# Kernel tuning notes

Measured on AMD Instinct MI355X. Metric: run time of the kernel, lower is better.

Reference implementation:

```python
import jax, jax.numpy as jnp
import numpy as np

N, E = 50000, 800000
D_IN, HID, H, C, E_DIM = 128, 128, 4, 32, 32  # C = HID // H


def setup_inputs() -> dict:
    key = jax.random.key(0)
    ks = jax.random.split(key, 16)
    def lin(k, fan_in, fan_out):
        return jax.random.normal(k, (fan_in, fan_out), jnp.float32) / np.sqrt(fan_in)
    return {
        "x": jax.random.normal(ks[0], (N, D_IN), jnp.float32),
        "edge_index": jax.random.randint(ks[1], (2, E), 0, N, jnp.int32),
        "edge_attr": jax.random.normal(ks[2], (E, E_DIM), jnp.float32),
        # TransformerConv params (bias=True on q/k/v and skip; lin_edge has no bias in PyG)
        "Wq": lin(ks[3], D_IN, HID), "bq": jnp.zeros((HID,), jnp.float32),
        "Wk": lin(ks[4], D_IN, HID), "bk": jnp.zeros((HID,), jnp.float32),
        "Wv": lin(ks[5], D_IN, HID), "bv": jnp.zeros((HID,), jnp.float32),
        "We": lin(ks[6], E_DIM, HID),
        "Wskip": lin(ks[7], D_IN, HID), "bskip": jnp.zeros((HID,), jnp.float32),
        # MLP([HID, HID, HID]) -> two Linear layers, GELU(tanh) after each (plain_last=False)
        "W1": lin(ks[8], HID, HID), "b1": jnp.zeros((HID,), jnp.float32),
        "W2": lin(ks[9], HID, HID), "b2": jnp.zeros((HID,), jnp.float32),
    }


def reference(x, edge_index, edge_attr, Wq, bq, Wk, bk, Wv, bv, We, Wskip, bskip, W1, b1, W2, b2):
    src, dst = edge_index[0], edge_index[1]  # messages flow src(j) -> dst(i)
    n = x.shape[0]
    q = (x @ Wq + bq).reshape(n, H, C)
    k = (x @ Wk + bk).reshape(n, H, C)
    v = (x @ Wv + bv).reshape(n, H, C)
    e = (edge_attr @ We).reshape(-1, H, C)          # [E,H,C]
    kj = k[src] + e                                  # gather + edge lift
    vj = v[src] + e
    alpha = jnp.einsum("ehc,ehc->eh", q[dst], kj) / np.sqrt(C)  # [E,H]
    # segment softmax over destination neighborhoods (PyG softmax semantics)
    amax = jax.ops.segment_max(alpha, dst, num_segments=n)      # [N,H]
    amax = jnp.where(jnp.isfinite(amax), amax, 0.0)
    ex = jnp.exp(alpha - amax[dst])
    denom = jax.ops.segment_sum(ex, dst, num_segments=n)
    alpha = ex / (denom[dst] + 1e-16)
    # (attention dropout p=0.3 is inactive in eval mode)
    agg = jax.ops.segment_sum(vj * alpha[:, :, None], dst, num_segments=n)  # [N,H,C]
    out = agg.reshape(n, HID) + (x @ Wskip + bskip)  # concat heads + root skip
    # residual MLP: gelu(tanh) after every layer since plain_last=False, norm=None
    h = jax.nn.gelu(out @ W1 + b1, approximate=True)
    h = jax.nn.gelu(h @ W2 + b2, approximate=True)
    return out + h
```

## Files before the change

### kernel.cpp

```cpp
#include <hip/hip_runtime.h>
#include <math.h>


#define D 128
#define EDIM 32

using bf16x8 = __attribute__((ext_vector_type(8))) short;
using f32x4  = __attribute__((ext_vector_type(4))) float;
using ushort8 = __attribute__((ext_vector_type(8))) unsigned short;
using v2h = __attribute__((ext_vector_type(2))) _Float16;

__device__ inline unsigned short f2bf(float f) {
    unsigned int u = __float_as_uint(f);
    u += 0x7FFFu + ((u >> 16) & 1u);
    return (unsigned short)(u >> 16);
}
__device__ inline float bf2f(unsigned short h) {
    return __uint_as_float(((unsigned int)h) << 16);
}
__device__ inline unsigned short f2h(float f) {
    union { _Float16 h; unsigned short u; } c;
    c.h = (_Float16)f;
    return c.u;
}
__device__ inline v2h u2h(unsigned int u) {
    union { unsigned int x; v2h h; } c; c.x = u; return c.h;
}
__device__ inline float gelu_fast(float x) {
    float x3 = x * x * x;
    float u = 0.7978845608028654f * (x + 0.044715f * x3);
    float t = 1.f - 2.f / (__expf(2.f * u) + 1.f);
    return 0.5f * x * (1.f + t);
}
__device__ inline float quad_add(float x) {
    int a = __builtin_amdgcn_update_dpp(0, __float_as_int(x), 0xB1, 0xF, 0xF, true);
    x += __int_as_float(a);
    a = __builtin_amdgcn_update_dpp(0, __float_as_int(x), 0x4E, 0xF, 0xF, true);
    x += __int_as_float(a);
    return x;
}

__device__ inline bf16x8 ldsB(const unsigned short* sw, int col, int kk0) {
    return *(const bf16x8*)(sw + col * 128 + (kk0 ^ ((col & 7) << 3)));
}

__global__ __launch_bounds__(256) void prep_kernel(
    const float* __restrict__ Wq, const float* __restrict__ Wk,
    const float* __restrict__ Wv, const float* __restrict__ Wsk,
    const float* __restrict__ W1, const float* __restrict__ W2,
    const float* __restrict__ We, const float* __restrict__ bq,
    unsigned short* __restrict__ Wt, float* __restrict__ bqE,
    const int* __restrict__ EI, int* __restrict__ deg, int E, int HB,
    const float* __restrict__ x, unsigned short* __restrict__ XB, long xtot)
{
    if ((int)blockIdx.x >= 513 + HB) {
        long i8 = ((long)(blockIdx.x - 513 - HB) * 256 + threadIdx.x) * 8;
        if (i8 + 8 <= xtot) {
            float4 a = *(const float4*)(x + i8);
            float4 b = *(const float4*)(x + i8 + 4);
            ushort8 u;
            u[0] = f2bf(a.x); u[1] = f2bf(a.y); u[2] = f2bf(a.z); u[3] = f2bf(a.w);
            u[4] = f2bf(b.x); u[5] = f2bf(b.y); u[6] = f2bf(b.z); u[7] = f2bf(b.w);
            *(ushort8*)(XB + i8) = u;
        }
        return;
    }
    if (blockIdx.x >= 513) {
        int e = (blockIdx.x - 513) * 256 + threadIdx.x;
        if (e < E) atomicAdd(&deg[EI[E + e]], 1);
        return;
    }
    int t = blockIdx.x * 256 + threadIdx.x;
    int m = t >> 14;
    int r = t & 16383;
    if (m >= 8) {
        if (r < 128) {
            const int hb = r & 96, k = r & 31;
            const float* wek = We + (size_t)k * D + hb;
            float s = 0.f;
#pragma unroll 8
            for (int c = 0; c < 32; ++c) s = fmaf(bq[hb + c], wek[c], s);
            bqE[r] = s;
        }
        return;
    }
    int col = r & 127, kk = r >> 7;
    float v;
    if (m < 6) {
        const float* W = (m == 0) ? Wq : (m == 1) ? Wk : (m == 2) ? Wv
                       : (m == 3) ? Wsk : (m == 4) ? W1 : W2;
        v = W[(size_t)kk * D + col];
    } else if (m == 6) {
        const int hb = col & 96;
        const float* wqr = Wq + (size_t)kk * D + hb;
        const float* wer = We + (size_t)(col & 31) * D + hb;
        float s = 0.f;
#pragma unroll 8
        for (int c = 0; c < 32; ++c) s = fmaf(wqr[c], wer[c], s);
        v = s;
    } else {
        v = ((kk >> 5) == (col >> 5)) ? We[(size_t)(kk & 31) * D + col] : 0.f;
    }
    Wt[(size_t)m * 16384 + (size_t)col * 128 + (kk ^ ((col & 7) << 3))] = f2bf(v);
}

__global__ __launch_bounds__(1024) void scanA(
    const int* __restrict__ deg, int* __restrict__ rowptr,
    int* __restrict__ psums, int N)
{
    __shared__ int tmp[1024];
    const int t = threadIdx.x;
    const int i = blockIdx.x * 1024 + t;
    int v = (i < N) ? deg[i] : 0;
    tmp[t] = v;
    __syncthreads();
    for (int off = 1; off < 1024; off <<= 1) {
        int add = (t >= off) ? tmp[t - off] : 0;
        __syncthreads();
        tmp[t] += add;
        __syncthreads();
    }
    if (i < N) rowptr[i + 1] = tmp[t];
    if (t == 1023) psums[blockIdx.x] = tmp[1023];
}

__global__ __launch_bounds__(1024) void scanB(int* __restrict__ psums, int nb)
{
    __shared__ int tmp[1024];
    const int t = threadIdx.x;
    int v = (t < nb) ? psums[t] : 0;
    tmp[t] = v;
    __syncthreads();
    for (int off = 1; off < 1024; off <<= 1) {
        int add = (t >= off) ? tmp[t - off] : 0;
        __syncthreads();
        tmp[t] += add;
        __syncthreads();
    }
    if (t < nb) psums[t] = tmp[t] - v;
}

__global__ __launch_bounds__(256) void scanC(
    int* __restrict__ rowptr, int* __restrict__ cursor,
    const int* __restrict__ psums, int N)
{
    int i = blockIdx.x * 256 + threadIdx.x;
    if (i == 0) { rowptr[0] = 0; cursor[0] = 0; }
    if (i < N) {
        int val = rowptr[i + 1] + psums[i >> 10];
        rowptr[i + 1] = val;
        if (i + 1 < N) cursor[i + 1] = val;
    }
}

__global__ __launch_bounds__(256) void scatter_ea(
    const int* __restrict__ EI, const float* __restrict__ EA,
    int* __restrict__ cursor, int2* __restrict__ SE,
    unsigned short* __restrict__ EAH, int E)
{
    int e = blockIdx.x * 256 + threadIdx.x;
    if (e >= E) return;
    int src = EI[e];
    int dst = EI[E + e];

    const float4* s4 = (const float4*)(EA + (size_t)e * EDIM);
    unsigned short* op = EAH + (size_t)e * EDIM;
#pragma unroll
    for (int j = 0; j < 4; ++j) {
        float4 a = s4[2 * j], b = s4[2 * j + 1];
        ushort8 u;
        u[0] = f2h(a.x); u[1] = f2h(a.y); u[2] = f2h(a.z); u[3] = f2h(a.w);
        u[4] = f2h(b.x); u[5] = f2h(b.y); u[6] = f2h(b.z); u[7] = f2h(b.w);
        *(ushort8*)(op + j * 8) = u;
    }

    int pos = atomicAdd(&cursor[dst], 1);
    SE[pos] = make_int2(src, e);
}

__global__ __launch_bounds__(256) void gemm5(
    const unsigned short* __restrict__ XB, const unsigned short* __restrict__ Wt,
    const float* __restrict__ bq, const float* __restrict__ bk,
    const float* __restrict__ bv, const float* __restrict__ bs,
    const float* __restrict__ bqE,
    unsigned short* __restrict__ QA, unsigned short* __restrict__ KV,
    float* __restrict__ S, int N, int NB2)
{
    __shared__ unsigned short sw[16384];
    const int t = threadIdx.x;
    const int bid = blockIdx.x;
    const int m = bid / NB2;
    const int bx = bid - m * NB2;
    const int widx = (m < 4) ? m : 6;
    const int lane = t & 63;
    const int w = t >> 6;
    const int row0 = bx * 128 + w * 32;
    const int lrow = lane & 15;
    const int kb = (lane >> 4) * 8;
    const int rq = (lane >> 4) * 4;

    const unsigned short* gsrc = Wt + (size_t)widx * 16384;
    ushort8 stg[8];
#pragma unroll
    for (int it = 0; it < 8; ++it)
        stg[it] = *(const ushort8*)(gsrc + (t + it * 256) * 8);

    bf16x8 af0[4], af1[4];
    {
        int a0 = row0 + lrow;      if (a0 > N - 1) a0 = N - 1;
        int a1 = row0 + 16 + lrow; if (a1 > N - 1) a1 = N - 1;
        const unsigned short* x0 = XB + (size_t)a0 * D + kb;
        const unsigned short* x1 = XB + (size_t)a1 * D + kb;
#pragma unroll
        for (int kf = 0; kf < 4; ++kf) {
            af0[kf] = *(const bf16x8*)(x0 + kf * 32);
            af1[kf] = *(const bf16x8*)(x1 + kf * 32);
        }
    }

#pragma unroll
    for (int it = 0; it < 8; ++it)
        *(ushort8*)(&sw[(t + it * 256) * 8]) = stg[it];
    __syncthreads();

    const float* bias = (m == 0) ? bq : (m == 1) ? bk : (m == 2) ? bv
                      : (m == 3) ? bs : bqE;
    f32x4 acc0[8], acc1[8];
#pragma unroll
    for (int nf = 0; nf < 8; ++nf) {
        acc0[nf] = (f32x4){0.f, 0.f, 0.f, 0.f};
        acc1[nf] = (f32x4){0.f, 0.f, 0.f, 0.f};
    }
#pragma unroll
    for (int nf = 0; nf < 8; ++nf) {
        const int col = nf * 16 + lrow;
#pragma unroll
        for (int kf = 0; kf < 4; ++kf) {
            bf16x8 bfr = ldsB(sw, col, kf * 32 + kb);
            acc0[nf] = __builtin_amdgcn_mfma_f32_16x16x32_bf16(af0[kf], bfr, acc0[nf], 0, 0, 0);
            acc1[nf] = __builtin_amdgcn_mfma_f32_16x16x32_bf16(af1[kf], bfr, acc1[nf], 0, 0, 0);
        }
    }

    if (m == 3) {
#pragma unroll
        for (int rb = 0; rb < 2; ++rb) {
#pragma unroll
            for (int nf = 0; nf < 8; ++nf) {
                const int col = nf * 16 + lrow;
                const float bb = bias[col];
#pragma unroll
                for (int i = 0; i < 4; ++i) {
                    int r = row0 + rb * 16 + rq + i;
                    if (r < N)
                        S[(size_t)r * D + col] = ((rb == 0) ? acc0[nf][i] : acc1[nf][i]) + bb;
                }
            }
        }
        return;
    }

    __syncthreads();
#pragma unroll
    for (int rb = 0; rb < 2; ++rb) {
#pragma unroll
        for (int nf = 0; nf < 8; ++nf) {
            const int col = nf * 16 + lrow;
            const float bb = bias[col];
#pragma unroll
            for (int i = 0; i < 4; ++i)
                sw[(w * 32 + rb * 16 + rq + i) * 128 + col] =
                    f2h(((rb == 0) ? acc0[nf][i] : acc1[nf][i]) + bb);
        }
    }
    unsigned short* gout = (m == 0) ? QA : (m == 1) ? KV
                         : (m == 2) ? KV + 128 : QA + 128;
#pragma unroll
    for (int it = 0; it < 8; ++it) {
        const int gidx = it * 64 + lane;
        const int row_l = gidx >> 4;
        const int chk = gidx & 15;
        const int r = row0 + row_l;
        ushort8 vv = *(const ushort8*)(&sw[(w * 32 + row_l) * 128 + chk * 8]);
        if (r < N) *(ushort8*)(gout + (size_t)r * 256 + chk * 8) = vv;
    }
}

__global__ __launch_bounds__(256) void gather_pass(
    const int* __restrict__ rowptr, const int2* __restrict__ SE,
    const unsigned short* __restrict__ EAH,
    const unsigned short* __restrict__ QA, const unsigned short* __restrict__ KV,
    float* __restrict__ SB, unsigned short* __restrict__ SAS, int N)
{
    const int lane = threadIdx.x & 63;
    const int wid = threadIdx.x >> 6;
    const int n = blockIdx.x * 4 + wid;
    if (n >= N) return;
    const int g = lane & 15;
    const int grp = lane >> 4;
    const int eoff = (g & 3) * 8;

    v2h q2[4], qe2[4];
    {
        uint4 qr  = *(const uint4*)(QA + (size_t)n * 256 + g * 8);
        uint4 qer = *(const uint4*)(QA + (size_t)n * 256 + 128 + g * 8);
        q2[0] = u2h(qr.x);  q2[1] = u2h(qr.y);  q2[2] = u2h(qr.z);  q2[3] = u2h(qr.w);
        qe2[0] = u2h(qer.x); qe2[1] = u2h(qer.y); qe2[2] = u2h(qer.z); qe2[3] = u2h(qer.w);
    }

    const v2h zero2 = {(_Float16)0.f, (_Float16)0.f};
    v2h acc2[4], sa2[4];
#pragma unroll
    for (int i = 0; i < 4; ++i) { acc2[i] = zero2; sa2[i] = zero2; }
    float den = 0.f;

    const int i0 = rowptr[n], i1 = rowptr[n + 1];

    int2 se[4];
#pragma unroll
    for (int u = 0; u < 4; ++u) {
        int ii = i0 + grp + u * 4;
        se[u] = (ii < i1) ? SE[ii] : make_int2(-1, 0);
    }

    for (int base = i0; base < i1; base += 16) {
        unsigned int kr[4][4], vr[4][4], er[4][4];
#pragma unroll
        for (int u = 0; u < 4; ++u) {
            if (se[u].x >= 0) {
                const unsigned short* kv = KV + (size_t)se[u].x * 256 + g * 8;
                *(uint4*)kr[u] = *(const uint4*)(kv);
                *(uint4*)vr[u] = *(const uint4*)(kv + 128);
                *(uint4*)er[u] = *(const uint4*)(EAH + (size_t)se[u].y * EDIM + eoff);
            } else {
                *(uint4*)kr[u] = (uint4){0, 0, 0, 0};
                *(uint4*)vr[u] = (uint4){0, 0, 0, 0};
                *(uint4*)er[u] = (uint4){0, 0, 0, 0};
            }
        }
        int2 seN[4];
#pragma unroll
        for (int u = 0; u < 4; ++u) {
            int ii = base + 16 + grp + u * 4;
            seN[u] = (ii < i1) ? SE[ii] : make_int2(-1, 0);
        }
#pragma unroll
        for (int u = 0; u < 4; ++u) {
            v2h ps = zero2;
#pragma unroll
            for (int i = 0; i < 4; ++i) {
                ps += q2[i]  * u2h(kr[u][i]);
                ps += qe2[i] * u2h(er[u][i]);
            }
            float p = (float)ps[0] + (float)ps[1];
            p = quad_add(p);
            const float ex = (se[u].x >= 0) ? __expf(p * 0.17677669529663689f) : 0.f;
            den += ex;
            const _Float16 exh = (_Float16)ex;
            const v2h ex2 = {exh, exh};
#pragma unroll
            for (int i = 0; i < 4; ++i) {
                acc2[i] += ex2 * u2h(vr[u][i]);
                sa2[i]  += ex2 * u2h(er[u][i]);
            }
        }
#pragma unroll
        for (int u = 0; u < 4; ++u) se[u] = seN[u];
    }

    float acc[8], sa[8];
#pragma unroll
    for (int i = 0; i < 4; ++i) {
        acc[2 * i] = (float)acc2[i][0]; acc[2 * i + 1] = (float)acc2[i][1];
        sa[2 * i]  = (float)sa2[i][0];  sa[2 * i + 1]  = (float)sa2[i][1];
    }
#pragma unroll
    for (int off = 16; off <= 32; off <<= 1) {
        den += __shfl_xor(den, off, 64);
#pragma unroll
        for (int j = 0; j < 8; ++j) {
            acc[j] += __shfl_xor(acc[j], off, 64);
            sa[j]  += __shfl_xor(sa[j],  off, 64);
        }
    }

    if (grp == 0) {
        const float rden = 1.f / (den + 1e-16f);
        float* so = SB + (size_t)n * D + g * 8;
        unsigned short* po = SAS + (size_t)n * D + g * 8;
#pragma unroll
        for (int j = 0; j < 8; ++j) {
            so[j] = fmaf(acc[j], rden, so[j]);
            po[j] = f2bf(sa[j] * rden);
        }
    }
}

__global__ __launch_bounds__(256) void fused_mlp(
    const float* __restrict__ SB, const unsigned short* __restrict__ SAS,
    const unsigned short* __restrict__ WtC, const unsigned short* __restrict__ Wt1,
    const unsigned short* __restrict__ Wt2,
    const float* __restrict__ b1, const float* __restrict__ b2,
    float* __restrict__ FINAL, int N)
{
    __shared__ unsigned short sw[16384];
    __shared__ unsigned short bounce[64 * 136];
    const int t = threadIdx.x;
    const int lane = t & 63;
    const int w = t >> 6;
    const int row0 = blockIdx.x * 64 + w * 16;
    const int lrow = lane & 15;
    const int kb = (lane >> 4) * 8;
    const int rq = (lane >> 4) * 4;

    ushort8 stg[8];
#pragma unroll
    for (int it = 0; it < 8; ++it)
        stg[it] = *(const ushort8*)(WtC + (t + it * 256) * 8);

    bf16x8 af[4];
    {
        int ar = row0 + lrow; if (ar > N - 1) ar = N - 1;
        const unsigned short* xr = SAS + (size_t)ar * D + kb;
#pragma unroll
        for (int kf = 0; kf < 4; ++kf) af[kf] = *(const bf16x8*)(xr + kf * 32);
    }
    f32x4 out[8];
#pragma unroll
    for (int nf = 0; nf < 8; ++nf) {
        const int col = nf * 16 + lrow;
#pragma unroll
        for (int i = 0; i < 4; ++i) {
            int r = row0 + rq + i;
            out[nf][i] = (r < N) ? SB[(size_t)r * D + col] : 0.f;
        }
    }
#pragma unroll
    for (int it = 0; it < 8; ++it)
        *(ushort8*)(&sw[(t + it * 256) * 8]) = stg[it];
    __syncthreads();

#pragma unroll
    for (int nf = 0; nf < 8; ++nf) {
        const int col = nf * 16 + lrow;
#pragma unroll
        for (int kf = 0; kf < 4; ++kf)
            out[nf] = __builtin_amdgcn_mfma_f32_16x16x32_bf16(
                af[kf], ldsB(sw, col, kf * 32 + kb), out[nf], 0, 0, 0);
    }
    __syncthreads();

#pragma unroll
    for (int it = 0; it < 8; ++it)
        stg[it] = *(const ushort8*)(Wt1 + (t + it * 256) * 8);
#pragma unroll
    for (int nf = 0; nf < 8; ++nf) {
        const int col = nf * 16 + lrow;
#pragma unroll
        for (int i = 0; i < 4; ++i)
            bounce[(w * 16 + rq + i) * 136 + col] = f2bf(out[nf][i]);
    }
#pragma unroll
    for (int it = 0; it < 8; ++it)
        *(ushort8*)(&sw[(t + it * 256) * 8]) = stg[it];
    __syncthreads();

    bf16x8 af2[4];
#pragma unroll
    for (int kf = 0; kf < 4; ++kf)
        af2[kf] = *(const bf16x8*)(&bounce[(w * 16 + lrow) * 136 + kb + kf * 32]);
    f32x4 acc2[8];
#pragma unroll
    for (int nf = 0; nf < 8; ++nf) acc2[nf] = (f32x4){0.f, 0.f, 0.f, 0.f};
#pragma unroll
    for (int nf = 0; nf < 8; ++nf) {
        const int col = nf * 16 + lrow;
#pragma unroll
        for (int kf = 0; kf < 4; ++kf)
            acc2[nf] = __builtin_amdgcn_mfma_f32_16x16x32_bf16(
                af2[kf], ldsB(sw, col, kf * 32 + kb), acc2[nf], 0, 0, 0);
    }
    __syncthreads();

#pragma unroll
    for (int it = 0; it < 8; ++it)
        stg[it] = *(const ushort8*)(Wt2 + (t + it * 256) * 8);
#pragma unroll
    for (int nf = 0; nf < 8; ++nf) {
        const int col = nf * 16 + lrow;
        const float bb = b1[col];
#pragma unroll
        for (int i = 0; i < 4; ++i)
            bounce[(w * 16 + rq + i) * 136 + col] = f2bf(gelu_fast(acc2[nf][i] + bb));
    }
#pragma unroll
    for (int it = 0; it < 8; ++it)
        *(ushort8*)(&sw[(t + it * 256) * 8]) = stg[it];
    __syncthreads();

    bf16x8 af3[4];
#pragma unroll
    for (int kf = 0; kf < 4; ++kf)
        af3[kf] = *(const bf16x8*)(&bounce[(w * 16 + lrow) * 136 + kb + kf * 32]);
    f32x4 acc3[8];
#pragma unroll
    for (int nf = 0; nf < 8; ++nf) acc3[nf] = (f32x4){0.f, 0.f, 0.f, 0.f};
#pragma unroll
    for (int nf = 0; nf < 8; ++nf) {
        const int col = nf * 16 + lrow;
#pragma unroll
        for (int kf = 0; kf < 4; ++kf)
            acc3[nf] = __builtin_amdgcn_mfma_f32_16x16x32_bf16(
                af3[kf], ldsB(sw, col, kf * 32 + kb), acc3[nf], 0, 0, 0);
    }
#pragma unroll
    for (int nf = 0; nf < 8; ++nf) {
        const int col = nf * 16 + lrow;
        const float bb = b2[col];
#pragma unroll
        for (int i = 0; i < 4; ++i) {
            int r = row0 + rq + i;
            if (r < N)
                FINAL[(size_t)r * D + col] = out[nf][i] + gelu_fast(acc3[nf][i] + bb);
        }
    }
}

extern "C" void kernel_launch(void* const* d_in, const int* in_sizes, int n_in,
                              void* d_out, int out_size, void* d_ws, size_t ws_size,
                              hipStream_t stream)
{
    const float* x   = (const float*)d_in[0];
    const int*   EI  = (const int*)  d_in[1];
    const float* EA  = (const float*)d_in[2];
    const float* Wq  = (const float*)d_in[3];
    const float* bq  = (const float*)d_in[4];
    const float* Wk  = (const float*)d_in[5];
    const float* bk  = (const float*)d_in[6];
    const float* Wv  = (const float*)d_in[7];
    const float* bv  = (const float*)d_in[8];
    const float* We  = (const float*)d_in[9];
    const float* Wsk = (const float*)d_in[10];
    const float* bsk = (const float*)d_in[11];
    const float* W1  = (const float*)d_in[12];
    const float* b1  = (const float*)d_in[13];
    const float* W2  = (const float*)d_in[14];
    const float* b2  = (const float*)d_in[15];

    const int N = in_sizes[0] / D;
    const int E = in_sizes[1] / 2;

    char* p = (char*)d_ws;
    auto alloc = [&](size_t bytes) -> void* {
        void* r = (void*)p;
        p += (bytes + 255) & ~(size_t)255;
        return r;
    };
    float*          Sb     = (float*)         alloc((size_t)N * D * 4);
    unsigned short* QAb    = (unsigned short*)alloc((size_t)N * 256 * 2);
    unsigned short* KVb    = (unsigned short*)alloc((size_t)N * 256 * 2);
    unsigned short* SASb   = (unsigned short*)alloc((size_t)N * D * 2);
    unsigned short* XBb    = (unsigned short*)alloc((size_t)N * D * 2);
    unsigned short* EAHb   = (unsigned short*)alloc((size_t)E * EDIM * 2);
    int2*           SEb    = (int2*)          alloc((size_t)E * 8);
    unsigned short* Wt     = (unsigned short*)alloc((size_t)8 * 16384 * 2);
    float*          bqEb   = (float*)         alloc((size_t)128 * 4);
    int*            deg    = (int*)           alloc((size_t)N * 4);
    int*            rowptr = (int*)           alloc((size_t)(N + 1) * 4);
    int*            cursor = (int*)           alloc((size_t)(N + 1) * 4);
    int*            psums  = (int*)           alloc((size_t)1024 * 4);

    hipMemsetAsync(deg, 0, (size_t)N * sizeof(int), stream);

    const long xtot = (long)N * D;
    const int NB  = (N + 63) / 64;
    const int NB2 = (N + 127) / 128;
    const int EB  = (E + 255) / 256;
    const int XB_ = (int)((xtot + 2047) / 2048);
    const int SB_ = (N + 1023) / 1024;

    prep_kernel<<<513 + EB + XB_, 256, 0, stream>>>(
        Wq, Wk, Wv, Wsk, W1, W2, We, bq, Wt, bqEb, EI, deg, E, EB, x, XBb, xtot);

    scanA<<<SB_, 1024, 0, stream>>>(deg, rowptr, psums, N);
    scanB<<<1, 1024, 0, stream>>>(psums, SB_);
    scanC<<<(N + 255) / 256, 256, 0, stream>>>(rowptr, cursor, psums, N);

    scatter_ea<<<EB, 256, 0, stream>>>(EI, EA, cursor, SEb, EAHb, E);

    gemm5<<<5 * NB2, 256, 0, stream>>>(
        XBb, Wt, bq, bk, bv, bsk, bqEb, QAb, KVb, Sb, N, NB2);

    gather_pass<<<(N + 3) / 4, 256, 0, stream>>>(
        rowptr, SEb, EAHb, QAb, KVb, Sb, SASb, N);

    fused_mlp<<<NB, 256, 0, stream>>>(Sb, SASb,
                                      Wt + (size_t)7 * 16384,
                                      Wt + (size_t)4 * 16384,
                                      Wt + (size_t)5 * 16384,
                                      b1, b2, (float*)d_out, N);
}
```

Before: 255.1 us.

## Move skip GEMM into MLP kernel and read fp32 edge attributes directly in gather

The root-skip projection moves out of the QKV GEMM launch and into the fused MLP kernel as an extra MFMA pass over XB, so the fp32 skip buffer is no longer written and re-read. The gather pass now writes its normalized aggregate as fp16 instead of accumulating into an fp32 buffer. Edge attributes are read as fp32 and converted to fp16 in registers, which drops the pre-converted fp16 edge-attribute copy from the scatter kernel. In exchange the gather reads twice as many edge-attribute bytes per edge, the MLP kernel does an extra 128x128 GEMM, and the aggregate loses precision by passing through fp16.

```diff
diff --git a/kernel.cpp b/kernel.cpp
--- a/kernel.cpp
+++ b/kernel.cpp
@@ -22,6 +22,11 @@
     union { _Float16 h; unsigned short u; } c;
     c.h = (_Float16)f;
     return c.u;
+}
+__device__ inline float h2f(unsigned short u) {
+    union { unsigned short u; _Float16 h; } c;
+    c.u = u;
+    return (float)c.h;
 }
 __device__ inline v2h u2h(unsigned int u) {
     union { unsigned int x; v2h h; } c; c.x = u; return c.h;
@@ -153,45 +158,31 @@
     }
 }
 
-__global__ __launch_bounds__(256) void scatter_ea(
-    const int* __restrict__ EI, const float* __restrict__ EA,
-    int* __restrict__ cursor, int2* __restrict__ SE,
-    unsigned short* __restrict__ EAH, int E)
+__global__ __launch_bounds__(256) void scatter_kernel(
+    const int* __restrict__ EI, int* __restrict__ cursor,
+    int2* __restrict__ SE, int E)
 {
     int e = blockIdx.x * 256 + threadIdx.x;
-    if (e >= E) return;
-    int src = EI[e];
-    int dst = EI[E + e];
-
-    const float4* s4 = (const float4*)(EA + (size_t)e * EDIM);
-    unsigned short* op = EAH + (size_t)e * EDIM;
-#pragma unroll
-    for (int j = 0; j < 4; ++j) {
-        float4 a = s4[2 * j], b = s4[2 * j + 1];
-        ushort8 u;
-        u[0] = f2h(a.x); u[1] = f2h(a.y); u[2] = f2h(a.z); u[3] = f2h(a.w);
-        u[4] = f2h(b.x); u[5] = f2h(b.y); u[6] = f2h(b.z); u[7] = f2h(b.w);
-        *(ushort8*)(op + j * 8) = u;
-    }
-
-    int pos = atomicAdd(&cursor[dst], 1);
-    SE[pos] = make_int2(src, e);
-}
-
-__global__ __launch_bounds__(256) void gemm5(
+    if (e < E) {
+        int dst = EI[E + e];
+        int pos = atomicAdd(&cursor[dst], 1);
+        SE[pos] = make_int2(EI[e], e);
+    }
+}
+
+__global__ __launch_bounds__(256) void gemm4(
     const unsigned short* __restrict__ XB, const unsigned short* __restrict__ Wt,
     const float* __restrict__ bq, const float* __restrict__ bk,
-    const float* __restrict__ bv, const float* __restrict__ bs,
-    const float* __restrict__ bqE,
+    const float* __restrict__ bv, const float* __restrict__ bqE,
     unsigned short* __restrict__ QA, unsigned short* __restrict__ KV,
-    float* __restrict__ S, int N, int NB2)
+    int N, int NB2)
 {
     __shared__ unsigned short sw[16384];
     const int t = threadIdx.x;
     const int bid = blockIdx.x;
     const int m = bid / NB2;
     const int bx = bid - m * NB2;
-    const int widx = (m < 4) ? m : 6;
+    const int widx = (m < 3) ? m : 6;
     const int lane = t & 63;
     const int w = t >> 6;
     const int row0 = bx * 128 + w * 32;
@@ -223,8 +214,7 @@
         *(ushort8*)(&sw[(t + it * 256) * 8]) = stg[it];
     __syncthreads();
 
-    const float* bias = (m == 0) ? bq : (m == 1) ? bk : (m == 2) ? bv
-                      : (m == 3) ? bs : bqE;
+    const float* bias = (m == 0) ? bq : (m == 1) ? bk : (m == 2) ? bv : bqE;
     f32x4 acc0[8], acc1[8];
 #pragma unroll
     for (int nf = 0; nf < 8; ++nf) {
@@ -240,24 +230,6 @@
             acc0[nf] = __builtin_amdgcn_mfma_f32_16x16x32_bf16(af0[kf], bfr, acc0[nf], 0, 0, 0);
             acc1[nf] = __builtin_amdgcn_mfma_f32_16x16x32_bf16(af1[kf], bfr, acc1[nf], 0, 0, 0);
         }
-    }
-
-    if (m == 3) {
-#pragma unroll
-        for (int rb = 0; rb < 2; ++rb) {
-#pragma unroll
-            for (int nf = 0; nf < 8; ++nf) {
-                const int col = nf * 16 + lrow;
-                const float bb = bias[col];
-#pragma unroll
-                for (int i = 0; i < 4; ++i) {
-                    int r = row0 + rb * 16 + rq + i;
-                    if (r < N)
-                        S[(size_t)r * D + col] = ((rb == 0) ? acc0[nf][i] : acc1[nf][i]) + bb;
-                }
-            }
-        }
-        return;
     }
 
     __syncthreads();
@@ -288,9 +260,9 @@
 
 __global__ __launch_bounds__(256) void gather_pass(
     const int* __restrict__ rowptr, const int2* __restrict__ SE,
-    const unsigned short* __restrict__ EAH,
+    const float* __restrict__ EA,
     const unsigned short* __restrict__ QA, const unsigned short* __restrict__ KV,
-    float* __restrict__ SB, unsigned short* __restrict__ SAS, int N)
+    unsigned short* __restrict__ PO, unsigned short* __restrict__ SAS, int N)
 {
     const int lane = threadIdx.x & 63;
     const int wid = threadIdx.x >> 6;
@@ -324,18 +296,22 @@
     }
 
     for (int base = i0; base < i1; base += 16) {
-        unsigned int kr[4][4], vr[4][4], er[4][4];
+        unsigned int kr[4][4], vr[4][4];
+        float4 e0[4], e1[4];
 #pragma unroll
         for (int u = 0; u < 4; ++u) {
             if (se[u].x >= 0) {
                 const unsigned short* kv = KV + (size_t)se[u].x * 256 + g * 8;
                 *(uint4*)kr[u] = *(const uint4*)(kv);
                 *(uint4*)vr[u] = *(const uint4*)(kv + 128);
-                *(uint4*)er[u] = *(const uint4*)(EAH + (size_t)se[u].y * EDIM + eoff);
+                const float* ear = EA + (size_t)se[u].y * EDIM + eoff;
+                e0[u] = *(const float4*)(ear);
+                e1[u] = *(const float4*)(ear + 4);
             } else {
                 *(uint4*)kr[u] = (uint4){0, 0, 0, 0};
                 *(uint4*)vr[u] = (uint4){0, 0, 0, 0};
-                *(uint4*)er[u] = (uint4){0, 0, 0, 0};
+                e0[u] = (float4){0.f, 0.f, 0.f, 0.f};
+                e1[u] = e0[u];
             }
         }
         int2 seN[4];
@@ -346,11 +322,16 @@
         }
 #pragma unroll
         for (int u = 0; u < 4; ++u) {
+            v2h e2[4];
+            e2[0] = (v2h){(_Float16)e0[u].x, (_Float16)e0[u].y};
+            e2[1] = (v2h){(_Float16)e0[u].z, (_Float16)e0[u].w};
+            e2[2] = (v2h){(_Float16)e1[u].x, (_Float16)e1[u].y};
+            e2[3] = (v2h){(_Float16)e1[u].z, (_Float16)e1[u].w};
             v2h ps = zero2;
 #pragma unroll
             for (int i = 0; i < 4; ++i) {
                 ps += q2[i]  * u2h(kr[u][i]);
-                ps += qe2[i] * u2h(er[u][i]);
+                ps += qe2[i] * e2[i];
             }
             float p = (float)ps[0] + (float)ps[1];
             p = quad_add(p);
@@ -361,7 +342,7 @@
 #pragma unroll
             for (int i = 0; i < 4; ++i) {
                 acc2[i] += ex2 * u2h(vr[u][i]);
-                sa2[i]  += ex2 * u2h(er[u][i]);
+                sa2[i]  += ex2 * e2[i];
             }
         }
 #pragma unroll
@@ -386,21 +367,23 @@
 
     if (grp == 0) {
         const float rden = 1.f / (den + 1e-16f);
-        float* so = SB + (size_t)n * D + g * 8;
-        unsigned short* po = SAS + (size_t)n * D + g * 8;
+        unsigned short* po = PO + (size_t)n * D + g * 8;
+        unsigned short* ps = SAS + (size_t)n * D + g * 8;
 #pragma unroll
         for (int j = 0; j < 8; ++j) {
-            so[j] = fmaf(acc[j], rden, so[j]);
-            po[j] = f2bf(sa[j] * rden);
+            po[j] = f2h(acc[j] * rden);
+            ps[j] = f2bf(sa[j] * rden);
         }
     }
 }
 
 __global__ __launch_bounds__(256) void fused_mlp(
-    const float* __restrict__ SB, const unsigned short* __restrict__ SAS,
-    const unsigned short* __restrict__ WtC, const unsigned short* __restrict__ Wt1,
-    const unsigned short* __restrict__ Wt2,
-    const float* __restrict__ b1, const float* __restrict__ b2,
+    const unsigned short* __restrict__ PO, const unsigned short* __restrict__ SAS,
+    const unsigned short* __restrict__ XB,
+    const unsigned short* __restrict__ WtC, const unsigned short* __restrict__ WtSk,
+    const unsigned short* __restrict__ Wt1, const unsigned short* __restrict__ Wt2,
+    const float* __restrict__ bsk, const float* __restrict__ b1,
+    const float* __restrict__ b2,
     float* __restrict__ FINAL, int N)
 {
     __shared__ unsigned short sw[16384];
@@ -412,6 +395,7 @@
     const int lrow = lane & 15;
     const int kb = (lane >> 4) * 8;
     const int rq = (lane >> 4) * 4;
+    const int ar = (row0 + lrow > N - 1) ? N - 1 : row0 + lrow;
 
     ushort8 stg[8];
 #pragma unroll
@@ -420,7 +404,6 @@
 
     bf16x8 af[4];
     {
-        int ar = row0 + lrow; if (ar > N - 1) ar = N - 1;
         const unsigned short* xr = SAS + (size_t)ar * D + kb;
 #pragma unroll
         for (int kf = 0; kf < 4; ++kf) af[kf] = *(const bf16x8*)(xr + kf * 32);
@@ -429,11 +412,35 @@
 #pragma unroll
     for (int nf = 0; nf < 8; ++nf) {
         const int col = nf * 16 + lrow;
+        const float bb = bsk[col];
 #pragma unroll
         for (int i = 0; i < 4; ++i) {
             int r = row0 + rq + i;
-            out[nf][i] = (r < N) ? SB[(size_t)r * D + col] : 0.f;
-        }
+            out[nf][i] = (r < N) ? h2f(PO[(size_t)r * D + col]) + bb : 0.f;
+        }
+    }
+#pragma unroll
+    for (int it = 0; it < 8; ++it)
+        *(ushort8*)(&sw[(t + it * 256) * 8]) = stg[it];
+    __syncthreads();
+
+#pragma unroll
+    for (int nf = 0; nf < 8; ++nf) {
+        const int col = nf * 16 + lrow;
+#pragma unroll
+        for (int kf = 0; kf < 4; ++kf)
+            out[nf] = __builtin_amdgcn_mfma_f32_16x16x32_bf16(
+                af[kf], ldsB(sw, col, kf * 32 + kb), out[nf], 0, 0, 0);
+    }
+    __syncthreads();
+
+#pragma unroll
+    for (int it = 0; it < 8; ++it)
+        stg[it] = *(const ushort8*)(WtSk + (t + it * 256) * 8);
+    {
+        const unsigned short* xr = XB + (size_t)ar * D + kb;
+#pragma unroll
+        for (int kf = 0; kf < 4; ++kf) af[kf] = *(const bf16x8*)(xr + kf * 32);
     }
 #pragma unroll
     for (int it = 0; it < 8; ++it)
@@ -556,12 +563,11 @@
         p += (bytes + 255) & ~(size_t)255;
         return r;
     };
-    float*          Sb     = (float*)         alloc((size_t)N * D * 4);
     unsigned short* QAb    = (unsigned short*)alloc((size_t)N * 256 * 2);
     unsigned short* KVb    = (unsigned short*)alloc((size_t)N * 256 * 2);
+    unsigned short* POb    = (unsigned short*)alloc((size_t)N * D * 2);
     unsigned short* SASb   = (unsigned short*)alloc((size_t)N * D * 2);
     unsigned short* XBb    = (unsigned short*)alloc((size_t)N * D * 2);
-    unsigned short* EAHb   = (unsigned short*)alloc((size_t)E * EDIM * 2);
     int2*           SEb    = (int2*)          alloc((size_t)E * 8);
     unsigned short* Wt     = (unsigned short*)alloc((size_t)8 * 16384 * 2);
     float*          bqEb   = (float*)         alloc((size_t)128 * 4);
@@ -586,17 +592,18 @@
     scanB<<<1, 1024, 0, stream>>>(psums, SB_);
     scanC<<<(N + 255) / 256, 256, 0, stream>>>(rowptr, cursor, psums, N);
 
-    scatter_ea<<<EB, 256, 0, stream>>>(EI, EA, cursor, SEb, EAHb, E);
-
-    gemm5<<<5 * NB2, 256, 0, stream>>>(
-        XBb, Wt, bq, bk, bv, bsk, bqEb, QAb, KVb, Sb, N, NB2);
+    scatter_kernel<<<EB, 256, 0, stream>>>(EI, cursor, SEb, E);
+
+    gemm4<<<4 * NB2, 256, 0, stream>>>(
+        XBb, Wt, bq, bk, bv, bqEb, QAb, KVb, N, NB2);
 
     gather_pass<<<(N + 3) / 4, 256, 0, stream>>>(
-        rowptr, SEb, EAHb, QAb, KVb, Sb, SASb, N);
-
-    fused_mlp<<<NB, 256, 0, stream>>>(Sb, SASb,
+        rowptr, SEb, EA, QAb, KVb, POb, SASb, N);
+
+    fused_mlp<<<NB, 256, 0, stream>>>(POb, SASb, XBb,
                                       Wt + (size_t)7 * 16384,
+                                      Wt + (size_t)3 * 16384,
                                       Wt + (size_t)4 * 16384,
                                       Wt + (size_t)5 * 16384,
-                                      b1, b2, (float*)d_out, N);
-}
+                                      bsk, b1, b2, (float*)d_out, N);
+}
```

Measured after the change: 262.0 us. 2.7% more time.
